# Optimization experiments

Measured on AMD Instinct MI355X. Metric: run time of the kernel, lower is better.

## Reference

```python
import jax, jax.numpy as jnp
import numpy as np

DIM = 192
NUM_HEADS = 6
WIN = (4, 4, 4)
SHIFT = (2, 2, 2)


def setup_inputs() -> dict:
    key = jax.random.key(0)
    k_x, k_qw, k_qb, k_pw, k_pb = jax.random.split(key, 5)
    C = DIM
    x = jax.random.normal(k_x, (1, C, 64, 64, 64), dtype=jnp.float32)
    lim = 1.0 / np.sqrt(C)
    qkv_w = jax.random.uniform(k_qw, (3 * C, C), minval=-lim, maxval=lim, dtype=jnp.float32)
    qkv_b = jax.random.uniform(k_qb, (3 * C,), minval=-lim, maxval=lim, dtype=jnp.float32)
    proj_w = jax.random.uniform(k_pw, (C, C), minval=-lim, maxval=lim, dtype=jnp.float32)
    proj_b = jax.random.uniform(k_pb, (C,), minval=-lim, maxval=lim, dtype=jnp.float32)
    return {"x": x, "qkv_w": qkv_w, "qkv_b": qkv_b, "proj_w": proj_w, "proj_b": proj_b}


def reference(x, qkv_w, qkv_b, proj_w, proj_b):
    B, C, X, Y, Z = x.shape
    Wx, Wy, Wz = WIN
    Sx, Sy, Sz = SHIFT
    H = NUM_HEADS
    hd = C // H
    scale = hd ** -0.5
    # cyclic shift
    x = jnp.roll(x, shift=(-Sx, -Sy, -Sz), axis=(2, 3, 4))
    nWx, nWy, nWz = X // Wx, Y // Wy, Z // Wz
    # window partition: (B,C,X,Y,Z) -> (B*nW, N_tok, C)
    h = x.reshape(B, C, nWx, Wx, nWy, Wy, nWz, Wz)
    h = jnp.transpose(h, (0, 2, 4, 6, 3, 5, 7, 1))  # (B,nWx,nWy,nWz,Wx,Wy,Wz,C)
    N_tok = Wx * Wy * Wz
    nW = B * nWx * nWy * nWz
    h = h.reshape(nW, N_tok, C)
    # qkv projection
    qkv = h @ qkv_w.T + qkv_b  # (nW, N, 3C)
    qkv = qkv.reshape(nW, N_tok, 3, H, hd)
    qkv = jnp.transpose(qkv, (2, 0, 3, 1, 4))  # (3, nW, H, N, hd)
    q, k, v = qkv[0], qkv[1], qkv[2]
    # scaled dot-product attention within each window
    attn = jnp.einsum('whqd,whkd->whqk', q, k) * scale
    attn = jax.nn.softmax(attn, axis=-1)
    out = jnp.einsum('whqk,whkd->whqd', attn, v)  # (nW, H, N, hd)
    out = jnp.transpose(out, (0, 2, 1, 3)).reshape(nW, N_tok, C)
    out = out @ proj_w.T + proj_b
    # window reverse: (nW, N, C) -> (B, C, X, Y, Z)
    out = out.reshape(B, nWx, nWy, nWz, Wx, Wy, Wz, C)
    out = jnp.transpose(out, (0, 7, 1, 4, 2, 5, 3, 6))
    out = out.reshape(B, C, X, Y, Z)
    out = jnp.roll(out, shift=(Sx, Sy, Sz), axis=(2, 3, 4))
    return out
```

## Files before the change

### kernel.cpp

```cpp
#include <hip/hip_runtime.h>
#include <stdint.h>

#define V_ELEMS (64*64*64)

typedef _Float16 f16x8 __attribute__((ext_vector_type(8)));
typedef _Float16 f16x4 __attribute__((ext_vector_type(4)));
typedef float f32x4 __attribute__((ext_vector_type(4)));

#define SMEM_BYTES 53248
#define H_STRIDE 200
#define QKP_STRIDE 72
#define VT_STRIDE 72
#define OH_STRIDE 72

__global__ void cvt_weights_kernel(const float* __restrict__ qkv_w,
                                   const float* __restrict__ proj_w,
                                   _Float16* __restrict__ w16) {
    int i = blockIdx.x * 256 + threadIdx.x;
    if (i < 110592)      w16[i] = (_Float16)qkv_w[i];
    else if (i < 147456) w16[i] = (_Float16)proj_w[i - 110592];
}

__global__ __launch_bounds__(256, 3)
void win_attn_kernel(const float* __restrict__ x,
                     const _Float16* __restrict__ w16,
                     const float* __restrict__ qkv_b,
                     const float* __restrict__ proj_b,
                     float* __restrict__ out)
{
    extern __shared__ char smem[];
    _Float16* h_s  = (_Float16*)smem;
    _Float16* qk_s = (_Float16*)(smem + 25600);
    _Float16* P_s  = (_Float16*)(smem + 25600);
    _Float16* vt_s = (_Float16*)(smem + 44032);
    _Float16* oh_s = (_Float16*)(smem + 44032);

    const _Float16* qw16 = w16;
    const _Float16* pw16 = w16 + 110592;

    const int tid  = threadIdx.x;
    const int wave = tid >> 6;
    const int lane = tid & 63;
    const int l15  = lane & 15;
    const int quad = lane >> 4;

    const int hh = (wave >> 1) & 1;
    const int dh = wave & 1;

    const int bid = blockIdx.x;
    const int xcd = bid & 7;
    const int s_  = bid >> 3;
    const int wzl = s_ & 3;
    const int gi  = (s_ >> 2) * 8 + xcd;
    const int wx  = gi >> 6;
    const int wy  = (gi >> 2) & 15;
    const int wz  = ((gi & 3) << 2) | wzl;

    {
        const int p  = tid & 1;
        const int r  = (tid >> 1) & 15;
        const int cb = tid >> 5;
        const int i = r >> 2, j = r & 3;
        const int xg = (wx*4 + i + 2) & 63;
        const int yg = (wy*4 + j + 2) & 63;
        const int zg = (wz*4 + 2 + 2*p) & 63;
        const int tok = r*4 + 2*p;
        const size_t sbase = ((size_t)xg*64 + (size_t)yg)*64 + (size_t)zg;
#pragma unroll
        for (int t = 0; t < 24; ++t) {
            int c = cb + 8*t;
            float2 v = *(const float2*)(x + (size_t)c*V_ELEMS + sbase);
            h_s[tok*H_STRIDE + c]     = (_Float16)v.x;
            h_s[(tok+1)*H_STRIDE + c] = (_Float16)v.y;
        }
    }

    f32x4 out_acc[3][4];
#pragma unroll
    for (int a = 0; a < 3; ++a)
#pragma unroll
        for (int b = 0; b < 4; ++b)
            out_acc[a][b] = (f32x4){0.f, 0.f, 0.f, 0.f};

    const f32x4 fzero = {0.f, 0.f, 0.f, 0.f};
    __syncthreads();

#pragma unroll
    for (int hp = 0; hp < 3; ++hp) {
        f16x8 bfr[3][6];
        float wbias[3];
#pragma unroll
        for (int wh = 0; wh < 3; ++wh) {
            const int n = wh*192 + (2*hp + hh)*32 + dh*16 + l15;
            wbias[wh] = qkv_b[n];
#pragma unroll
            for (int ks = 0; ks < 6; ++ks)
                bfr[wh][ks] = *(const f16x8*)(qw16 + (size_t)n*192 + ks*32 + quad*8);
        }
        __builtin_amdgcn_s_setprio(1);
#pragma unroll
        for (int rt = 0; rt < 4; ++rt) {
            f16x8 af[6];
#pragma unroll
            for (int ks = 0; ks < 6; ++ks)
                af[ks] = *(const f16x8*)(h_s + (rt*16 + l15)*H_STRIDE + ks*32 + quad*8);
#pragma unroll
            for (int wh = 0; wh < 3; ++wh) {
                f32x4 acc = fzero;
#pragma unroll
                for (int ks = 0; ks < 6; ++ks)
                    acc = __builtin_amdgcn_mfma_f32_16x16x32_f16(af[ks], bfr[wh][ks], acc, 0, 0, 0);
                if (wh == 2) {
                    f16x4 pk;
#pragma unroll
                    for (int r2 = 0; r2 < 4; ++r2) pk[r2] = (_Float16)(acc[r2] + wbias[2]);
                    *(f16x4*)(vt_s + (hh*32 + dh*16 + l15)*VT_STRIDE + rt*16 + quad*4) = pk;
                } else {
                    _Float16* dst = qk_s + hh*64*QKP_STRIDE + (wh == 1 ? 32 : 0);
#pragma unroll
                    for (int r2 = 0; r2 < 4; ++r2)
                        dst[(rt*16 + quad*4 + r2)*QKP_STRIDE + dh*16 + l15] =
                            (_Float16)(acc[r2] + wbias[wh]);
                }
            }
        }
        __builtin_amdgcn_s_setprio(0);
        __syncthreads();

        f32x4 pfr[2][4];
        float inv_r[2][4];
#pragma unroll
        for (int jj = 0; jj < 2; ++jj) {
            f16x8 aq = *(const f16x8*)(qk_s + (jj*64 + wave*16 + l15)*QKP_STRIDE + quad*8);
            f32x4 s[4];
#pragma unroll
            for (int ct = 0; ct < 4; ++ct) {
                f16x8 bk = *(const f16x8*)(qk_s + (jj*64 + ct*16 + l15)*QKP_STRIDE + 32 + quad*8);
                s[ct] = __builtin_amdgcn_mfma_f32_16x16x32_f16(aq, bk, fzero, 0, 0, 0);
            }
            float mx[4];
#pragma unroll
            for (int r = 0; r < 4; ++r) {
                float m = fmaxf(fmaxf(s[0][r], s[1][r]), fmaxf(s[2][r], s[3][r]));
#pragma unroll
                for (int msk = 1; msk < 16; msk <<= 1) m = fmaxf(m, __shfl_xor(m, msk));
                mx[r] = m;
            }
            const float kscale = 0.17677669529663687f * 1.4426950408889634f;
#pragma unroll
            for (int ct = 0; ct < 4; ++ct)
#pragma unroll
                for (int r = 0; r < 4; ++r)
                    s[ct][r] = exp2f((s[ct][r] - mx[r]) * kscale);
#pragma unroll
            for (int r = 0; r < 4; ++r) {
                float sum = s[0][r] + s[1][r] + s[2][r] + s[3][r];
#pragma unroll
                for (int msk = 1; msk < 16; msk <<= 1) sum += __shfl_xor(sum, msk);
                inv_r[jj][r] = 1.0f / sum;
            }
#pragma unroll
            for (int ct = 0; ct < 4; ++ct) pfr[jj][ct] = s[ct];
        }
        __syncthreads();

#pragma unroll
        for (int jj = 0; jj < 2; ++jj)
#pragma unroll
            for (int ct = 0; ct < 4; ++ct)
#pragma unroll
                for (int r = 0; r < 4; ++r)
                    P_s[(jj*64 + wave*16 + quad*4 + r)*QKP_STRIDE + ct*16 + l15] =
                        (_Float16)pfr[jj][ct][r];

        f32x4 oacc[2][2];
#pragma unroll
        for (int jj = 0; jj < 2; ++jj)
#pragma unroll
            for (int ct = 0; ct < 2; ++ct) oacc[jj][ct] = fzero;
#pragma unroll
        for (int jj = 0; jj < 2; ++jj)
#pragma unroll
            for (int ks = 0; ks < 2; ++ks) {
                f16x8 ap = *(const f16x8*)(P_s + (jj*64 + wave*16 + l15)*QKP_STRIDE + ks*32 + quad*8);
#pragma unroll
                for (int ct = 0; ct < 2; ++ct) {
                    f16x8 bv = *(const f16x8*)(vt_s + (jj*32 + ct*16 + l15)*VT_STRIDE + ks*32 + quad*8);
                    oacc[jj][ct] = __builtin_amdgcn_mfma_f32_16x16x32_f16(ap, bv, oacc[jj][ct], 0, 0, 0);
                }
            }
        __syncthreads();

#pragma unroll
        for (int jj = 0; jj < 2; ++jj)
#pragma unroll
            for (int ct = 0; ct < 2; ++ct)
#pragma unroll
                for (int r = 0; r < 4; ++r)
                    oh_s[(wave*16 + quad*4 + r)*OH_STRIDE + jj*32 + ct*16 + l15] =
                        (_Float16)(oacc[jj][ct][r] * inv_r[jj][r]);
        __syncthreads();

        f16x8 afr[4][2];
#pragma unroll
        for (int rt = 0; rt < 4; ++rt)
#pragma unroll
            for (int ks = 0; ks < 2; ++ks)
                afr[rt][ks] = *(const f16x8*)(oh_s + (rt*16 + l15)*OH_STRIDE + ks*32 + quad*8);
        __builtin_amdgcn_s_setprio(1);
#pragma unroll
        for (int cti = 0; cti < 3; ++cti) {
            const int n = (wave + 4*cti)*16 + l15;
#pragma unroll
            for (int ks = 0; ks < 2; ++ks) {
                f16x8 bf = *(const f16x8*)(pw16 + (size_t)n*192 + hp*64 + ks*32 + quad*8);
#pragma unroll
                for (int rt = 0; rt < 4; ++rt)
                    out_acc[cti][rt] =
                        __builtin_amdgcn_mfma_f32_16x16x32_f16(afr[rt][ks], bf, out_acc[cti][rt], 0, 0, 0);
            }
        }
        __builtin_amdgcn_s_setprio(0);
        __syncthreads();
    }

    {
        const int zA = wz*4 + 2;
        const int zB = (wz*4 + 4) & 63;
        const int yg = (wy*4 + quad + 2) & 63;
#pragma unroll
        for (int cti = 0; cti < 3; ++cti) {
            const int n = (wave + 4*cti)*16 + l15;
            const float bias = proj_b[n];
#pragma unroll
            for (int rt = 0; rt < 4; ++rt) {
                const int xg = (wx*4 + rt + 2) & 63;
                const size_t base = (((size_t)n*64 + (size_t)xg)*64 + (size_t)yg)*64;
                float2 v01 = { out_acc[cti][rt][0] + bias, out_acc[cti][rt][1] + bias };
                float2 v23 = { out_acc[cti][rt][2] + bias, out_acc[cti][rt][3] + bias };
                *(float2*)(out + base + zA) = v01;
                *(float2*)(out + base + zB) = v23;
            }
        }
    }
}

extern "C" void kernel_launch(void* const* d_in, const int* in_sizes, int n_in,
                              void* d_out, int out_size, void* d_ws, size_t ws_size,
                              hipStream_t stream) {
    const float* x      = (const float*)d_in[0];
    const float* qkv_w  = (const float*)d_in[1];
    const float* qkv_b  = (const float*)d_in[2];
    const float* proj_w = (const float*)d_in[3];
    const float* proj_b = (const float*)d_in[4];
    float* out = (float*)d_out;
    _Float16* w16 = (_Float16*)d_ws;

    cvt_weights_kernel<<<dim3(576), dim3(256), 0, stream>>>(qkv_w, proj_w, w16);
    win_attn_kernel<<<dim3(4096), dim3(256), SMEM_BYTES, stream>>>(
        x, w16, qkv_b, proj_b, out);
}
```

Before: 688.3 us.

## Split window gather and scatter into separate coalesced kernels via workspace

Adds a gather kernel that reads x with coalesced float4 loads, converts it to fp16, and writes window-contiguous token rows to a workspace buffer. A scatter kernel reads window-ordered fp32 attention output, adds the bias, and writes the output with coalesced float4 stores. The attention kernel now loads and stores contiguous workspace rows instead of doing strided global access. The aim is to replace the strided 2-element accesses in the fused kernel, at the cost of roughly 300MB of extra workspace traffic and two more launches. The original fused path is kept as a fallback when the workspace is too small.

```diff
diff --git a/kernel.cpp b/kernel.cpp
--- a/kernel.cpp
+++ b/kernel.cpp
@@ -12,6 +12,10 @@
 #define QKP_STRIDE 72
 #define VT_STRIDE 72
 #define OH_STRIDE 72
+
+#define W16_BYTES  294912
+#define HWS_BYTES  100663296
+#define OWS_BYTES  201326592
 
 __global__ void cvt_weights_kernel(const float* __restrict__ qkv_w,
                                    const float* __restrict__ proj_w,
@@ -21,12 +25,75 @@
     else if (i < 147456) w16[i] = (_Float16)proj_w[i - 110592];
 }
 
+__global__ __launch_bounds__(256, 6)
+void gather_kernel(const float* __restrict__ x, _Float16* __restrict__ hws) {
+    __shared__ _Float16 L[64 * 200];
+    const int xg = blockIdx.x >> 6, yg = blockIdx.x & 63;
+    const int tid = threadIdx.x;
+
+    {
+        const int zq = tid & 15, cb = tid >> 4;
+#pragma unroll
+        for (int u = 0; u < 12; ++u) {
+            const int c = cb + 16 * u;
+            const float4 v = *(const float4*)(x + ((size_t)c * 4096 + (size_t)xg * 64 + yg) * 64 + zq * 4);
+            const int z0 = zq * 4;
+            L[(z0 + 0) * 200 + c] = (_Float16)v.x;
+            L[(z0 + 1) * 200 + c] = (_Float16)v.y;
+            L[(z0 + 2) * 200 + c] = (_Float16)v.z;
+            L[(z0 + 3) * 200 + c] = (_Float16)v.w;
+        }
+    }
+    __syncthreads();
+
+    const int tx = (xg + 62) & 63, wx = tx >> 2, i = tx & 3;
+    const int ty = (yg + 62) & 63, wy = ty >> 2, j = ty & 3;
+    const int wz  = tid & 15;
+    const int zl  = (tid >> 4) & 3;
+    const int c8b = tid >> 6;
+    const int zg  = (wz * 4 + 2 + zl) & 63;
+    const size_t base = (size_t)((wx * 16 + wy) * 16 + wz) * 12288 + (size_t)(i * 16 + j * 4 + zl) * 192;
+#pragma unroll
+    for (int u = 0; u < 6; ++u) {
+        const int c8 = c8b + 4 * u;
+        f16x8 v = *(const f16x8*)(L + zg * 200 + c8 * 8);
+        *(f16x8*)(hws + base + c8 * 8) = v;
+    }
+}
+
+__global__ __launch_bounds__(256, 8)
+void scatter_kernel(const float* __restrict__ ows, const float* __restrict__ proj_b,
+                    float* __restrict__ out) {
+    const uint32_t g = blockIdx.x * 256 + threadIdx.x;
+    const int zq = g & 15;
+    const int yg = (g >> 4) & 63;
+    const int xg = (g >> 10) & 63;
+    const int c  = g >> 16;
+    const int tx = (xg + 62) & 63, wx = tx >> 2, i = tx & 3;
+    const int ty = (yg + 62) & 63, wy = ty >> 2, j = ty & 3;
+    const float bias = proj_b[c];
+    float4 v;
+    float* vp = (float*)&v;
+#pragma unroll
+    for (int k = 0; k < 4; ++k) {
+        const int a  = (zq * 4 + k + 62) & 63;
+        const int wz = a >> 2, zl = a & 3;
+        const size_t idx = (size_t)((wx * 16 + wy) * 16 + wz) * 12288
+                         + (size_t)(i * 16 + j * 4 + zl) * 192 + c;
+        vp[k] = ows[idx] + bias;
+    }
+    *(float4*)(out + ((size_t)c * 4096 + (size_t)xg * 64 + yg) * 64 + zq * 4) = v;
+}
+
+template<int GWS, int SWS>
 __global__ __launch_bounds__(256, 3)
 void win_attn_kernel(const float* __restrict__ x,
                      const _Float16* __restrict__ w16,
                      const float* __restrict__ qkv_b,
                      const float* __restrict__ proj_b,
-                     float* __restrict__ out)
+                     float* __restrict__ out,
+                     const _Float16* __restrict__ hws,
+                     float* __restrict__ ows)
 {
     extern __shared__ char smem[];
     _Float16* h_s  = (_Float16*)smem;
@@ -55,8 +122,18 @@
     const int wx  = gi >> 6;
     const int wy  = (gi >> 2) & 15;
     const int wz  = ((gi & 3) << 2) | wzl;
-
-    {
+    const int W   = (wx * 16 + wy) * 16 + wz;
+
+    if (GWS) {
+        const size_t wbase = (size_t)W * 12288;
+        const int row = tid >> 2, part = tid & 3;
+#pragma unroll
+        for (int u = 0; u < 6; ++u) {
+            const int c8 = part + 4 * u;
+            f16x8 v = *(const f16x8*)(hws + wbase + (size_t)row * 192 + c8 * 8);
+            *(f16x8*)(h_s + row * H_STRIDE + c8 * 8) = v;
+        }
+    } else {
         const int p  = tid & 1;
         const int r  = (tid >> 1) & 15;
         const int cb = tid >> 5;
@@ -224,7 +301,18 @@
         __syncthreads();
     }
 
-    {
+    if (SWS) {
+        const size_t obase = (size_t)W * 12288;
+#pragma unroll
+        for (int cti = 0; cti < 3; ++cti) {
+            const int n = (wave + 4*cti)*16 + l15;
+#pragma unroll
+            for (int rt = 0; rt < 4; ++rt)
+#pragma unroll
+                for (int r = 0; r < 4; ++r)
+                    ows[obase + (size_t)(rt*16 + quad*4 + r)*192 + n] = out_acc[cti][rt][r];
+        }
+    } else {
         const int zA = wz*4 + 2;
         const int zB = (wz*4 + 4) & 63;
         const int yg = (wy*4 + quad + 2) & 63;
@@ -254,9 +342,25 @@
     const float* proj_w = (const float*)d_in[3];
     const float* proj_b = (const float*)d_in[4];
     float* out = (float*)d_out;
-    _Float16* w16 = (_Float16*)d_ws;
+    char* wsb = (char*)d_ws;
+    _Float16* w16 = (_Float16*)wsb;
 
     cvt_weights_kernel<<<dim3(576), dim3(256), 0, stream>>>(qkv_w, proj_w, w16);
-    win_attn_kernel<<<dim3(4096), dim3(256), SMEM_BYTES, stream>>>(
-        x, w16, qkv_b, proj_b, out);
-}
+
+    if (ws_size >= (size_t)W16_BYTES + HWS_BYTES + OWS_BYTES) {
+        _Float16* hws = (_Float16*)(wsb + W16_BYTES);
+        float*    ows = (float*)(wsb + W16_BYTES + HWS_BYTES);
+        gather_kernel<<<dim3(4096), dim3(256), 0, stream>>>(x, hws);
+        win_attn_kernel<1,1><<<dim3(4096), dim3(256), SMEM_BYTES, stream>>>(
+            x, w16, qkv_b, proj_b, out, hws, ows);
+        scatter_kernel<<<dim3(49152), dim3(256), 0, stream>>>(ows, proj_b, out);
+    } else if (ws_size >= (size_t)W16_BYTES + OWS_BYTES) {
+        float* ows = (float*)(wsb + W16_BYTES);
+        win_attn_kernel<0,1><<<dim3(4096), dim3(256), SMEM_BYTES, stream>>>(
+            x, w16, qkv_b, proj_b, out, (const _Float16*)nullptr, ows);
+        scatter_kernel<<<dim3(49152), dim3(256), 0, stream>>>(ows, proj_b, out);
+    } else {
+        win_attn_kernel<0,0><<<dim3(4096), dim3(256), SMEM_BYTES, stream>>>(
+            x, w16, qkv_b, proj_b, out, (const _Float16*)nullptr, (float*)nullptr);
+    }
+}
```

Result: slower. 940.6 us (+36.7%).
